# Kernel optimization log

Hardware: AMD Instinct MI355X
Metric: run time of the kernel (lower is better)

Reference implementation:

```python
import jax, jax.numpy as jnp
import numpy as np

MIN_GAP = 5
MIN_SIZE = 5
# max_size defaults to inf, so the upper bound min(i+MAX_SIZE, T) is just T


def setup_inputs() -> dict:
    key = jax.random.key(0)
    k1, k2 = jax.random.split(key)
    B, T = 8, 4096
    w_phi = jax.random.normal(k1, (B, 1, T), dtype=jnp.float32)
    # target onset/offset frame indices in [0, T)
    y = jax.random.uniform(k2, (B, 2), dtype=jnp.float32) * T
    return {"w_phi": w_phi, "y": y, "eps": 5}


def reference(w_phi, y, eps):
    B, _, T = w_phi.shape
    x = w_phi[:, 0, :]  # [B, T] per-frame scores
    idx = jnp.arange(T, dtype=x.dtype)
    # hinge penalties: max(0, |y0 - i| - eps), max(0, |y1 - j| - eps)
    pi = jnp.maximum(0.0, jnp.abs(y[:, 0:1] - idx) - eps)  # [B, T]
    pj = jnp.maximum(0.0, jnp.abs(y[:, 1:2] - idx) - eps)  # [B, T]
    # score(i, j) = x[i] + x[j] + (pi[i] + pj[j]) / 2 = a[i] + b[j]
    a = x + 0.5 * pi  # onset part
    b = x + 0.5 * pj  # offset part
    ii = jnp.arange(T)
    # valid pairs: i >= MIN_GAP and j >= i + MIN_SIZE (j < T implicit)
    mask = (ii[:, None] >= MIN_GAP) & (ii[None, :] >= ii[:, None] + MIN_SIZE)
    scores = a[:, :, None] + b[:, None, :]  # [B, T, T]
    neg = jnp.finfo(scores.dtype).min
    best = jnp.max(jnp.where(mask[None], scores, neg), axis=(1, 2))  # [B]
    # initial candidate: onset=1, offset=1+MIN_SIZE (kept if strictly greatest)
    init = a[:, 1] + b[:, 1 + MIN_SIZE]
    out = jnp.maximum(best, init)
    return jnp.mean(out)  # loss summed over batch / batch_size
```

## Files before the change

kernel.cpp:

```cpp
#include <hip/hip_runtime.h>

#define T 4096
#define B 8
#define CHUNK 64
#define MIN_GAP 5
#define MIN_SIZE 5
#define NEG (-3.402823466e38f)

__global__ __launch_bounds__(512, 2)
void custom_loss_kernel(const float* __restrict__ w_phi,
                        const float* __restrict__ y,
                        const int* __restrict__ eps_p,
                        float* __restrict__ out) {
    const int t    = threadIdx.x;
    const int wave = t >> 6;
    const int lane = t & 63;

    const float eps = (float)eps_p[0];
    const float y0  = y[wave * 2 + 0];
    const float y1  = y[wave * 2 + 1];
    const float* __restrict__ x = w_phi + (size_t)wave * T + (size_t)lane * CHUNK;

    __shared__ float wred[B];

    float xr[CHUNK];
    #pragma unroll
    for (int q = 0; q < CHUNK / 4; q++) {
        float4 v = ((const float4*)x)[q];
        xr[4 * q + 0] = v.x;
        xr[4 * q + 1] = v.y;
        xr[4 * q + 2] = v.z;
        xr[4 * q + 3] = v.w;
    }

    const float base = (float)(lane * CHUNK);

    float ls[CHUNK];
    {
        float run = NEG;
        #pragma unroll
        for (int j = CHUNK - 1; j >= 0; j--) {
            float fj = base + (float)j;
            float bj = xr[j] + 0.5f * fmaxf(0.0f, fabsf(y1 - fj) - eps);
            run = fmaxf(run, bj);
            ls[j] = run;
        }
    }

    float inc = ls[0];
    #pragma unroll
    for (int off = 1; off < 64; off <<= 1) {
        float u = __shfl_down(inc, off, 64);
        inc = (lane + off < 64) ? fmaxf(inc, u) : inc;
    }
    float S = __shfl_down(inc, 1, 64);
    if (lane == 63) S = NEG;

    float nsm[MIN_SIZE];
    #pragma unroll
    for (int k = 0; k < MIN_SIZE; k++) {
        nsm[k] = __shfl_down(fmaxf(ls[k], S), 1, 64);
    }

    float best = NEG;
    #pragma unroll
    for (int j = 0; j < CHUNK; j++) {
        float fj = base + (float)j;
        float aj = xr[j] + 0.5f * fmaxf(0.0f, fabsf(y0 - fj) - eps);
        float smv;
        bool valid;
        if (j <= CHUNK - 1 - MIN_SIZE) {
            smv   = fmaxf(ls[j + MIN_SIZE], S);
            valid = true;
        } else {
            smv   = nsm[j - (CHUNK - MIN_SIZE)];
            valid = (lane < 63);
        }
        if (lane == 0 && j < MIN_GAP) valid = false;
        if (valid) best = fmaxf(best, aj + smv);
    }

    #pragma unroll
    for (int off = 32; off > 0; off >>= 1) {
        best = fmaxf(best, __shfl_down(best, off, 64));
    }

    if (lane == 0) {
        float a1 = xr[1] + 0.5f * fmaxf(0.0f, fabsf(y0 - 1.0f) - eps);
        float b6 = xr[6] + 0.5f * fmaxf(0.0f, fabsf(y1 - (float)(1 + MIN_SIZE)) - eps);
        wred[wave] = fmaxf(best, a1 + b6);
    }
    __syncthreads();

    if (t == 0) {
        float s = 0.0f;
        #pragma unroll
        for (int k = 0; k < B; k++) s += wred[k];
        out[0] = s * 0.125f;
    }
}

extern "C" void kernel_launch(void* const* d_in, const int* in_sizes, int n_in,
                              void* d_out, int out_size, void* d_ws, size_t ws_size,
                              hipStream_t stream) {
    const float* w_phi = (const float*)d_in[0];
    const float* y     = (const float*)d_in[1];
    const int*   eps   = (const int*)d_in[2];
    float* out = (float*)d_out;

    custom_loss_kernel<<<1, 512, 0, stream>>>(w_phi, y, eps, out);
}
```

Measured before the change: 62.02 us.

## Split batch across blocks with per-block cross-wave suffix max and combine kernel

Rather than one block in which each wave handles a whole batch row of 64 elements per lane, the work now runs as one block per batch row. Each thread takes 8 elements, and a suffix max is carried across waves through shared memory. A second tiny kernel averages the per-batch partials. This spreads the latency-bound serial per-lane work over 8 CUs and cuts the per-thread chain length. In exchange it adds an extra kernel launch, workspace traffic and a couple of block-level barriers.

```diff
diff --git a/kernel.cpp b/kernel.cpp
--- a/kernel.cpp
+++ b/kernel.cpp
@@ -2,38 +2,41 @@
 
 #define T 4096
 #define B 8
-#define CHUNK 64
+#define WAVES 8
+#define THREADS (WAVES * 64)
+#define CHUNK 8
 #define MIN_GAP 5
 #define MIN_SIZE 5
 #define NEG (-3.402823466e38f)
 
-__global__ __launch_bounds__(512, 2)
-void custom_loss_kernel(const float* __restrict__ w_phi,
-                        const float* __restrict__ y,
-                        const int* __restrict__ eps_p,
-                        float* __restrict__ out) {
+__global__ __launch_bounds__(THREADS, 2)
+void custom_loss_batch(const float* __restrict__ w_phi,
+                       const float* __restrict__ y,
+                       const int* __restrict__ eps_p,
+                       float* __restrict__ partial) {
+    const int bat  = blockIdx.x;
     const int t    = threadIdx.x;
     const int wave = t >> 6;
     const int lane = t & 63;
 
     const float eps = (float)eps_p[0];
-    const float y0  = y[wave * 2 + 0];
-    const float y1  = y[wave * 2 + 1];
-    const float* __restrict__ x = w_phi + (size_t)wave * T + (size_t)lane * CHUNK;
+    const float y0  = y[bat * 2 + 0];
+    const float y1  = y[bat * 2 + 1];
+    const float* __restrict__ x = w_phi + (size_t)bat * T + (size_t)t * CHUNK;
 
-    __shared__ float wred[B];
+    __shared__ float wmax[WAVES];
+    __shared__ float nxt0[WAVES][MIN_SIZE];
+    __shared__ float wbest[WAVES];
 
     float xr[CHUNK];
-    #pragma unroll
-    for (int q = 0; q < CHUNK / 4; q++) {
-        float4 v = ((const float4*)x)[q];
-        xr[4 * q + 0] = v.x;
-        xr[4 * q + 1] = v.y;
-        xr[4 * q + 2] = v.z;
-        xr[4 * q + 3] = v.w;
+    {
+        float4 v0 = ((const float4*)x)[0];
+        float4 v1 = ((const float4*)x)[1];
+        xr[0] = v0.x; xr[1] = v0.y; xr[2] = v0.z; xr[3] = v0.w;
+        xr[4] = v1.x; xr[5] = v1.y; xr[6] = v1.z; xr[7] = v1.w;
     }
 
-    const float base = (float)(lane * CHUNK);
+    const float base = (float)(t * CHUNK);
 
     float ls[CHUNK];
     {
@@ -56,27 +59,48 @@
     float S = __shfl_down(inc, 1, 64);
     if (lane == 63) S = NEG;
 
+    if (lane == 0) wmax[wave] = inc;
+    __syncthreads();
+
+    float W = NEG;
+    #pragma unroll
+    for (int w2 = 0; w2 < WAVES; w2++) {
+        if (w2 > wave) W = fmaxf(W, wmax[w2]);
+    }
+    const float SW = fmaxf(S, W);
+
+    if (lane == 0) {
+        #pragma unroll
+        for (int k = 0; k < MIN_SIZE; k++)
+            nxt0[wave][k] = fmaxf(ls[k], SW);
+    }
+
     float nsm[MIN_SIZE];
     #pragma unroll
     for (int k = 0; k < MIN_SIZE; k++) {
-        nsm[k] = __shfl_down(fmaxf(ls[k], S), 1, 64);
+        nsm[k] = __shfl_down(fmaxf(ls[k], SW), 1, 64);
+    }
+    __syncthreads();
+    if (lane == 63 && wave < WAVES - 1) {
+        #pragma unroll
+        for (int k = 0; k < MIN_SIZE; k++) nsm[k] = nxt0[wave + 1][k];
     }
 
     float best = NEG;
+    const bool lastLane = (wave == WAVES - 1) && (lane == 63);
     #pragma unroll
     for (int j = 0; j < CHUNK; j++) {
         float fj = base + (float)j;
         float aj = xr[j] + 0.5f * fmaxf(0.0f, fabsf(y0 - fj) - eps);
         float smv;
-        bool valid;
+        bool valid = true;
         if (j <= CHUNK - 1 - MIN_SIZE) {
-            smv   = fmaxf(ls[j + MIN_SIZE], S);
-            valid = true;
+            smv = fmaxf(ls[j + MIN_SIZE], SW);
         } else {
             smv   = nsm[j - (CHUNK - MIN_SIZE)];
-            valid = (lane < 63);
+            valid = !lastLane;
         }
-        if (lane == 0 && j < MIN_GAP) valid = false;
+        if (t == 0 && j < MIN_GAP) valid = false;
         if (valid) best = fmaxf(best, aj + smv);
     }
 
@@ -84,18 +108,25 @@
     for (int off = 32; off > 0; off >>= 1) {
         best = fmaxf(best, __shfl_down(best, off, 64));
     }
-
-    if (lane == 0) {
-        float a1 = xr[1] + 0.5f * fmaxf(0.0f, fabsf(y0 - 1.0f) - eps);
-        float b6 = xr[6] + 0.5f * fmaxf(0.0f, fabsf(y1 - (float)(1 + MIN_SIZE)) - eps);
-        wred[wave] = fmaxf(best, a1 + b6);
-    }
+    if (lane == 0) wbest[wave] = best;
     __syncthreads();
 
     if (t == 0) {
+        float r = wbest[0];
+        #pragma unroll
+        for (int w2 = 1; w2 < WAVES; w2++) r = fmaxf(r, wbest[w2]);
+        float a1 = xr[1] + 0.5f * fmaxf(0.0f, fabsf(y0 - 1.0f) - eps);
+        float b6 = xr[6] + 0.5f * fmaxf(0.0f, fabsf(y1 - (float)(1 + MIN_SIZE)) - eps);
+        partial[bat] = fmaxf(r, a1 + b6);
+    }
+}
+
+__global__ void custom_loss_combine(const float* __restrict__ partial,
+                                    float* __restrict__ out) {
+    if (threadIdx.x == 0) {
         float s = 0.0f;
         #pragma unroll
-        for (int k = 0; k < B; k++) s += wred[k];
+        for (int k = 0; k < B; k++) s += partial[k];
         out[0] = s * 0.125f;
     }
 }
@@ -106,7 +137,9 @@
     const float* w_phi = (const float*)d_in[0];
     const float* y     = (const float*)d_in[1];
     const int*   eps   = (const int*)d_in[2];
-    float* out = (float*)d_out;
+    float* out     = (float*)d_out;
+    float* partial = (float*)d_ws;
 
-    custom_loss_kernel<<<1, 512, 0, stream>>>(w_phi, y, eps, out);
+    custom_loss_batch<<<B, THREADS, 0, stream>>>(w_phi, y, eps, partial);
+    custom_loss_combine<<<1, 64, 0, stream>>>(partial, out);
 }
```

Result: faster. 58.36 us (-5.9%).
